# Kernel optimization log

Measured on AMD Instinct MI355X. Metric: run time of the kernel, lower is better.

Reference implementation:

```python
import jax, jax.numpy as jnp
import numpy as np
from jax import lax

POOL = 4  # hp['gcn_pool_size']


def sparsemax(z):
    # sparsemax along last axis (Martins & Astudillo 2016), matches tfa.activations.sparsemax
    n = z.shape[-1]
    z_sorted = jnp.flip(jnp.sort(z, axis=-1), axis=-1)          # descending
    k = jnp.arange(1, n + 1, dtype=z.dtype)
    zcum = jnp.cumsum(z_sorted, axis=-1)
    support = (1.0 + k * z_sorted) > zcum                        # [.., n] bool
    k_sel = jnp.sum(support, axis=-1, keepdims=True)             # int, >= 1
    tau = (jnp.take_along_axis(zcum, k_sel - 1, axis=-1) - 1.0) / k_sel.astype(z.dtype)
    return jnp.maximum(z - tau, 0.0)


def gcn_layer(x, W):
    # x: [B, T, E]
    T = x.shape[1]
    # einsum('Bte,bte->tBb') then mean over t == contract over t,e and divide by T
    adj = jnp.einsum('Bte,bte->Bb', x, x) / T                    # [B, B]
    adj = sparsemax(adj)                                         # row-wise sparsemax
    m = adj[:, :, None, None] * x[None]                          # [B, b, T, E] outer product
    # MaxPool2D((POOL,1), stride 1, 'same') on [batch=B, H=b, W=T, C=E]: pool over neighbor axis b
    m = lax.reduce_window(m, -jnp.inf, lax.max,
                          (1, POOL, 1, 1), (1, 1, 1, 1), 'SAME')
    agg = jnp.sum(m, axis=1)                                     # [B, T, E]
    return jax.nn.relu(agg @ W)                                  # [B, T, rel_dim]


def setup_inputs() -> dict:
    key = jax.random.key(0)
    k0, k1, k2, k3 = jax.random.split(key, 4)
    B, T, E = 64, 256, 64
    rel_dim, n_stack = 4, 8
    x = jax.random.normal(k0, (B, T, E), dtype=jnp.float32)
    W0 = jax.random.normal(k1, (E, rel_dim), dtype=jnp.float32) * 0.1
    W1 = jax.random.normal(k2, (rel_dim, rel_dim), dtype=jnp.float32) * 0.1
    Wp = jax.random.normal(k3, (rel_dim, n_stack), dtype=jnp.float32) * 0.1
    return {"x": x, "W0": W0, "W1": W1, "Wp": Wp}


def reference(x, W0, W1, Wp):
    x = gcn_layer(x, W0)           # layer 0: E -> rel_dim
    x = gcn_layer(x, W1)           # layer 1: rel_dim -> rel_dim
    pooled = jnp.mean(x, axis=1)   # [B, rel_dim], mean over T
    return jax.nn.softmax(pooled @ Wp, axis=-1)  # [B, n_stack]
```

## Files before the change

### kernel.cpp

```cpp
#include <hip/hip_runtime.h>
#include <math.h>

__device__ __forceinline__ float4 f4max(float4 a, float4 b) {
    return make_float4(fmaxf(a.x, b.x), fmaxf(a.y, b.y), fmaxf(a.z, b.z), fmaxf(a.w, b.w));
}
__device__ __forceinline__ float4 f4scale(float s, float4 v) {
    return make_float4(s * v.x, s * v.y, s * v.z, s * v.w);
}
__device__ __forceinline__ float4 f4add(float4 a, float4 b) {
    return make_float4(a.x + b.x, a.y + b.y, a.z + b.z, a.w + b.w);
}
__device__ __forceinline__ float4 f4fma(float a, float4 b, float4 c) {
    return make_float4(fmaf(a, b.x, c.x), fmaf(a, b.y, c.y), fmaf(a, b.z, c.z), fmaf(a, b.w, c.w));
}
__device__ __forceinline__ float4 f4fma4(float4 a, float4 b, float4 c) {
    return make_float4(fmaf(a.x, b.x, c.x), fmaf(a.y, b.y, c.y),
                       fmaf(a.z, b.z, c.z), fmaf(a.w, b.w, c.w));
}

__device__ __forceinline__ float wave_sparsemax(float z, int lane) {
    float v = z;
    for (int k = 2; k <= 64; k <<= 1) {
        bool desc = (lane & k) == 0;
        for (int j = k >> 1; j > 0; j >>= 1) {
            float other = __shfl_xor(v, j, 64);
            bool lower = (lane & j) == 0;
            float mn = fminf(v, other), mx = fmaxf(v, other);
            v = (desc ^ lower) ? mn : mx;
        }
    }
    float c = v;
    for (int d = 1; d < 64; d <<= 1) {
        float n = __shfl_up(c, d, 64);
        if (lane >= d) c += n;
    }
    bool sup = (1.0f + (float)(lane + 1) * v) > c;
    int ksel = __popcll(__ballot(sup));
    float zk = __shfl(c, ksel - 1, 64);
    float tau = (zk - 1.0f) / (float)ksel;
    return fmaxf(z - tau, 0.f);
}

__global__ __launch_bounds__(256)
void gram0_kernel(const float* __restrict__ X, float* __restrict__ adjraw) {
    __shared__ float xsT[64][68];
    int tid = threadIdx.x;
    int k0 = blockIdx.x * 64;
#pragma unroll
    for (int it = 0; it < 4; ++it) {
        int f = it * 256 + tid;
        int i = f >> 4, k4 = (f & 15) * 4;
        float4 v = *(const float4*)(X + (size_t)i * 16384 + k0 + k4);
        xsT[k4 + 0][i] = v.x; xsT[k4 + 1][i] = v.y;
        xsT[k4 + 2][i] = v.z; xsT[k4 + 3][i] = v.w;
    }
    __syncthreads();
    int ti = (tid >> 4) * 4, tj = (tid & 15) * 4;
    float4 a0 = make_float4(0, 0, 0, 0), a1 = a0, a2 = a0, a3 = a0;
#pragma unroll 8
    for (int k = 0; k < 64; ++k) {
        float4 a = *(const float4*)&xsT[k][ti];
        float4 b = *(const float4*)&xsT[k][tj];
        a0 = f4fma(a.x, b, a0); a1 = f4fma(a.y, b, a1);
        a2 = f4fma(a.z, b, a2); a3 = f4fma(a.w, b, a3);
    }
    float* r0 = adjraw + (ti + 0) * 64 + tj;
    float* r1 = adjraw + (ti + 1) * 64 + tj;
    float* r2 = adjraw + (ti + 2) * 64 + tj;
    float* r3 = adjraw + (ti + 3) * 64 + tj;
    atomicAdd(r0 + 0, a0.x); atomicAdd(r0 + 1, a0.y); atomicAdd(r0 + 2, a0.z); atomicAdd(r0 + 3, a0.w);
    atomicAdd(r1 + 0, a1.x); atomicAdd(r1 + 1, a1.y); atomicAdd(r1 + 2, a1.z); atomicAdd(r1 + 3, a1.w);
    atomicAdd(r2 + 0, a2.x); atomicAdd(r2 + 1, a2.y); atomicAdd(r2 + 2, a2.z); atomicAdd(r2 + 3, a2.w);
    atomicAdd(r3 + 0, a3.x); atomicAdd(r3 + 1, a3.y); atomicAdd(r3 + 2, a3.z); atomicAdd(r3 + 3, a3.w);
}

__global__ __launch_bounds__(256)
void agg0_kernel(const float* __restrict__ x, const float* __restrict__ adjraw,
                 const float* __restrict__ W0, float* __restrict__ h0) {
    __shared__ float psm[8 * 64];
    int tid = threadIdx.x;
    int lane = tid & 63;
    int w = __builtin_amdgcn_readfirstlane(tid >> 6);
    int t0 = (blockIdx.x >> 3) * 4;
    int Bc = (blockIdx.x & 7) * 8;
    {
        float zA = adjraw[(Bc + 2 * w) * 64 + lane] * (1.0f / 256.0f);
        float zB = adjraw[(Bc + 2 * w + 1) * 64 + lane] * (1.0f / 256.0f);
        psm[(2 * w) * 64 + lane] = wave_sparsemax(zA, lane);
        psm[(2 * w + 1) * 64 + lane] = wave_sparsemax(zB, lane);
    }
    int t = lane >> 4, eq = lane & 15;
    const float* pA = psm + (2 * w) * 64;
    const float* pB = pA + 64;
    float4 w0r0 = *(const float4*)(W0 + (eq * 4 + 0) * 4);
    float4 w0r1 = *(const float4*)(W0 + (eq * 4 + 1) * 4);
    float4 w0r2 = *(const float4*)(W0 + (eq * 4 + 2) * 4);
    float4 w0r3 = *(const float4*)(W0 + (eq * 4 + 3) * 4);
    const float4* xg = (const float4*)(x + ((size_t)(t0 + t) * 64) + eq * 4);
    float4 x4 = xg[0];
    float4 vA = f4scale(pA[0], x4), vB = f4scale(pB[0], x4);
    float4 qm1A = vA, qm1B = vB;
    x4 = xg[4096];
    float4 vtA = f4scale(pA[1], x4), vtB = f4scale(pB[1], x4);
    float4 qbA = f4max(vA, vtA), qbB = f4max(vB, vtB);
    float4 accA = make_float4(0, 0, 0, 0), accB = accA;
#pragma unroll 8
    for (int bl = 0; bl < 62; ++bl) {
        x4 = xg[(size_t)(bl + 2) * 4096];
        float4 vnA = f4scale(pA[bl + 2], x4);
        float4 vnB = f4scale(pB[bl + 2], x4);
        float4 q1A = f4max(vtA, vnA), q1B = f4max(vtB, vnB);
        accA = f4add(accA, f4max(qm1A, q1A));
        accB = f4add(accB, f4max(qm1B, q1B));
        qm1A = qbA; qbA = q1A; vtA = vnA;
        qm1B = qbB; qbB = q1B; vtB = vnB;
    }
    accA = f4add(accA, f4max(qm1A, vtA));
    accB = f4add(accB, f4max(qm1B, vtB));
    accA = f4add(accA, qbA);
    accB = f4add(accB, qbB);
#pragma unroll
    for (int half = 0; half < 2; ++half) {
        float4 acc = half ? accB : accA;
        float4 h = f4fma(acc.x, w0r0, f4fma(acc.y, w0r1,
                   f4fma(acc.z, w0r2, f4scale(acc.w, w0r3))));
        for (int m = 1; m <= 8; m <<= 1) {
            h.x += __shfl_xor(h.x, m, 64);
            h.y += __shfl_xor(h.y, m, 64);
            h.z += __shfl_xor(h.z, m, 64);
            h.w += __shfl_xor(h.w, m, 64);
        }
        if (eq == 0) {
            int B = Bc + 2 * w + half;
            float4 r = make_float4(fmaxf(h.x, 0.f), fmaxf(h.y, 0.f),
                                   fmaxf(h.z, 0.f), fmaxf(h.w, 0.f));
            *(float4*)(h0 + (size_t)(B * 256 + t0 + t) * 4) = r;
        }
    }
}

__global__ __launch_bounds__(256)
void tail_kernel(const float* __restrict__ h0, const float* __restrict__ W1,
                 const float* __restrict__ Wp, float* __restrict__ out) {
    __shared__ __align__(16) float row[4 * 260];
    __shared__ float part[256];
    __shared__ float psm[64];
    __shared__ float red[16];
    int tid = threadIdx.x;
    int lane = tid & 63;
    int bid = blockIdx.x;
    {
        int q = tid >> 6, s = (tid & 63) * 4;
        *(float4*)(row + q * 260 + s) = *(const float4*)(h0 + (size_t)bid * 1024 + tid * 4);
    }
    __syncthreads();
    {
        int j = tid >> 2, q = tid & 3;
        const float4* hj = (const float4*)(h0 + (size_t)j * 1024 + q * 256);
        const float4* ri = (const float4*)(row + q * 260);
        float4 s4 = make_float4(0, 0, 0, 0);
#pragma unroll 8
        for (int kk = 0; kk < 64; ++kk) s4 = f4fma4(ri[kk], hj[kk], s4);
        part[tid] = s4.x + s4.y + s4.z + s4.w;
    }
    __syncthreads();
    if (tid < 64) {
        float z = (part[lane * 4] + part[lane * 4 + 1] + part[lane * 4 + 2]
                   + part[lane * 4 + 3]) * (1.0f / 256.0f);
        psm[lane] = wave_sparsemax(z, lane);
    }
    __syncthreads();
    int w = __builtin_amdgcn_readfirstlane(tid >> 6);
    int rc = lane & 3;
    float psum = 0.f;
#pragma unroll
    for (int gg = 0; gg < 4; ++gg) {
        int tbase = w * 64 + gg * 16;
        const float* xb = h0 + (size_t)tbase * 4 + lane;
        float v0 = psm[0] * xb[0];
        float v1 = psm[1] * xb[1024];
        float qm1 = v0, qb = fmaxf(v0, v1), vt = v1, acc = 0.f;
#pragma unroll 8
        for (int bl = 0; bl < 62; ++bl) {
            float vn = psm[bl + 2] * xb[(size_t)(bl + 2) * 1024];
            float q1 = fmaxf(vt, vn);
            acc += fmaxf(qm1, q1);
            qm1 = qb; qb = q1; vt = vn;
        }
        acc += fmaxf(qm1, vt);
        acc += qb;
        int base = lane & ~3;
        float b0 = __shfl(acc, base + 0, 64);
        float b1 = __shfl(acc, base + 1, 64);
        float b2 = __shfl(acc, base + 2, 64);
        float b3 = __shfl(acc, base + 3, 64);
        float h = b0 * W1[rc] + b1 * W1[4 + rc] + b2 * W1[8 + rc] + b3 * W1[12 + rc];
        psum += fmaxf(h, 0.f);
    }
    for (int m = 4; m <= 32; m <<= 1) psum += __shfl_xor(psum, m, 64);
    if (lane < 4) red[w * 4 + lane] = psum;
    __syncthreads();
    if (tid < 64) {
        float pooled = 0.f;
        if (lane < 4)
            pooled = (red[lane] + red[4 + lane] + red[8 + lane] + red[12 + lane])
                     * (1.0f / 256.0f);
        float q0 = __shfl(pooled, 0, 64), q1 = __shfl(pooled, 1, 64);
        float q2 = __shfl(pooled, 2, 64), q3 = __shfl(pooled, 3, 64);
        float logit = -INFINITY;
        if (lane < 8)
            logit = q0 * Wp[lane] + q1 * Wp[8 + lane]
                  + q2 * Wp[16 + lane] + q3 * Wp[24 + lane];
        float mx = logit;
        for (int m = 4; m >= 1; m >>= 1) mx = fmaxf(mx, __shfl_xor(mx, m, 8));
        float e = (lane < 8) ? __expf(logit - mx) : 0.f;
        float s = e;
        for (int m = 4; m >= 1; m >>= 1) s += __shfl_xor(s, m, 8);
        if (lane < 8) out[bid * 8 + lane] = e / s;
    }
}

extern "C" void kernel_launch(void* const* d_in, const int* in_sizes, int n_in,
                              void* d_out, int out_size, void* d_ws, size_t ws_size,
                              hipStream_t stream) {
    const float* x  = (const float*)d_in[0];
    const float* W0 = (const float*)d_in[1];
    const float* W1 = (const float*)d_in[2];
    const float* Wp = (const float*)d_in[3];
    float* out = (float*)d_out;

    char* ws = (char*)d_ws;
    float* adjraw = (float*)ws;
    float* h0     = (float*)(ws + 16384);

    hipMemsetAsync(adjraw, 0, 16384, stream);
    gram0_kernel<<<256, 256, 0, stream>>>(x, adjraw);
    agg0_kernel<<<512, 256, 0, stream>>>(x, adjraw, W0, h0);
    tail_kernel<<<64, 256, 0, stream>>>(h0, W1, Wp, out);
}
```

Before: 130.9 us.

## Replace atomic Gram accumulation with partial buffers and a separate reduce+sparsemax kernel

The Gram kernel now writes each block's 64x64 partial into its own slice of a 4 MB workspace instead of issuing float atomicAdds, so the memset goes away. A new reduce kernel sums the 256 partials per row and applies sparsemax once per row. The aggregation kernel then reads the precomputed sparsemax weights directly, which removes the redundant per-block sparsemax work. The cost is 4 MB of extra global write and read traffic and one more kernel launch.

```diff
diff --git a/kernel.cpp b/kernel.cpp
--- a/kernel.cpp
+++ b/kernel.cpp
@@ -42,7 +42,7 @@
 }
 
 __global__ __launch_bounds__(256)
-void gram0_kernel(const float* __restrict__ X, float* __restrict__ adjraw) {
+void gram_partial(const float* __restrict__ X, float* __restrict__ P) {
     __shared__ float xsT[64][68];
     int tid = threadIdx.x;
     int k0 = blockIdx.x * 64;
@@ -64,33 +64,42 @@
         a0 = f4fma(a.x, b, a0); a1 = f4fma(a.y, b, a1);
         a2 = f4fma(a.z, b, a2); a3 = f4fma(a.w, b, a3);
     }
-    float* r0 = adjraw + (ti + 0) * 64 + tj;
-    float* r1 = adjraw + (ti + 1) * 64 + tj;
-    float* r2 = adjraw + (ti + 2) * 64 + tj;
-    float* r3 = adjraw + (ti + 3) * 64 + tj;
-    atomicAdd(r0 + 0, a0.x); atomicAdd(r0 + 1, a0.y); atomicAdd(r0 + 2, a0.z); atomicAdd(r0 + 3, a0.w);
-    atomicAdd(r1 + 0, a1.x); atomicAdd(r1 + 1, a1.y); atomicAdd(r1 + 2, a1.z); atomicAdd(r1 + 3, a1.w);
-    atomicAdd(r2 + 0, a2.x); atomicAdd(r2 + 1, a2.y); atomicAdd(r2 + 2, a2.z); atomicAdd(r2 + 3, a2.w);
-    atomicAdd(r3 + 0, a3.x); atomicAdd(r3 + 1, a3.y); atomicAdd(r3 + 2, a3.z); atomicAdd(r3 + 3, a3.w);
-}
-
-__global__ __launch_bounds__(256)
-void agg0_kernel(const float* __restrict__ x, const float* __restrict__ adjraw,
+    float* basep = P + ((size_t)blockIdx.x << 12);
+    *(float4*)(basep + (ti + 0) * 64 + tj) = a0;
+    *(float4*)(basep + (ti + 1) * 64 + tj) = a1;
+    *(float4*)(basep + (ti + 2) * 64 + tj) = a2;
+    *(float4*)(basep + (ti + 3) * 64 + tj) = a3;
+}
+
+__global__ __launch_bounds__(256)
+void reduce_sm(const float* __restrict__ P, float* __restrict__ adj0) {
+    __shared__ float red[4 * 64];
+    int tid = threadIdx.x;
+    int row = blockIdx.x;
+    int w = tid >> 6;
+    int lane = tid & 63;
+    float s = 0.f;
+    for (int c = w * 64; c < (w + 1) * 64; ++c)
+        s += P[((size_t)c << 12) + row * 64 + lane];
+    red[w * 64 + lane] = s;
+    __syncthreads();
+    if (tid < 64) {
+        float z = (red[lane] + red[64 + lane] + red[128 + lane] + red[192 + lane])
+                  * (1.0f / 256.0f);
+        adj0[row * 64 + lane] = wave_sparsemax(z, lane);
+    }
+}
+
+__global__ __launch_bounds__(256)
+void agg0_kernel(const float* __restrict__ x, const float* __restrict__ adj0,
                  const float* __restrict__ W0, float* __restrict__ h0) {
-    __shared__ float psm[8 * 64];
     int tid = threadIdx.x;
     int lane = tid & 63;
     int w = __builtin_amdgcn_readfirstlane(tid >> 6);
     int t0 = (blockIdx.x >> 3) * 4;
     int Bc = (blockIdx.x & 7) * 8;
-    {
-        float zA = adjraw[(Bc + 2 * w) * 64 + lane] * (1.0f / 256.0f);
-        float zB = adjraw[(Bc + 2 * w + 1) * 64 + lane] * (1.0f / 256.0f);
-        psm[(2 * w) * 64 + lane] = wave_sparsemax(zA, lane);
-        psm[(2 * w + 1) * 64 + lane] = wave_sparsemax(zB, lane);
-    }
     int t = lane >> 4, eq = lane & 15;
-    const float* pA = psm + (2 * w) * 64;
+    const float* pA = adj0 + (Bc + 2 * w) * 64;
     const float* pB = pA + 64;
     float4 w0r0 = *(const float4*)(W0 + (eq * 4 + 0) * 4);
     float4 w0r1 = *(const float4*)(W0 + (eq * 4 + 1) * 4);
@@ -230,11 +239,12 @@
     float* out = (float*)d_out;
 
     char* ws = (char*)d_ws;
-    float* adjraw = (float*)ws;
-    float* h0     = (float*)(ws + 16384);
-
-    hipMemsetAsync(adjraw, 0, 16384, stream);
-    gram0_kernel<<<256, 256, 0, stream>>>(x, adjraw);
-    agg0_kernel<<<512, 256, 0, stream>>>(x, adjraw, W0, h0);
+    float* P    = (float*)ws;
+    float* adj0 = (float*)(ws + (4u << 20));
+    float* h0   = (float*)(ws + (4u << 20) + 16384);
+
+    gram_partial<<<256, 256, 0, stream>>>(x, P);
+    reduce_sm<<<64, 256, 0, stream>>>(P, adj0);
+    agg0_kernel<<<512, 256, 0, stream>>>(x, adj0, W0, h0);
     tail_kernel<<<64, 256, 0, stream>>>(h0, W1, Wp, out);
 }
```

Result: faster. 118.8 us (-9.2%).
